# Kernel optimization log

Hardware: AMD Instinct MI355X
Metric: run time of the kernel (lower is better)

## Reference

```python
import jax, jax.numpy as jnp
import numpy as np

B = 1024
IN_Q = 2048
IN_KV = 2048
NH = 16
D = 64
INNER = NH * D
TF = 4
NC = 2
EPS = 1e-5
SLOPE = 0.01  # LeakyReLU default negative slope


def setup_inputs() -> dict:
    key = jax.random.key(0)
    ks = jax.random.split(key, 8)
    s = 0.02
    return {
        "q_input": jax.random.normal(ks[0], (B, IN_Q), jnp.float32),
        "kv_input": jax.random.normal(ks[1], (B, IN_KV), jnp.float32),
        "Wq": jax.random.normal(ks[2], (INNER, IN_Q), jnp.float32) * s,
        "bq": jax.random.normal(ks[3], (INNER,), jnp.float32) * s,
        "Wkv": jax.random.normal(ks[4], (2 * INNER, IN_KV), jnp.float32) * s,
        "bkv": jax.random.normal(ks[5], (2 * INNER,), jnp.float32) * s,
        "bn_w": jnp.ones((TF,), jnp.float32),
        "bn_b": jnp.zeros((TF,), jnp.float32),
        "Wo": jax.random.normal(ks[6], (NC, TF), jnp.float32) * s,
        "bo": jax.random.normal(ks[7], (NC,), jnp.float32) * s,
    }


def reference(q_input, kv_input, Wq, bq, Wkv, bkv, bn_w, bn_b, Wo, bo):
    b = q_input.shape[0]
    # projections: [B, NH, D] and [B, NH, 2D]
    q = (q_input @ Wq.T + bq).reshape(b, NH, D)
    kv = (kv_input @ Wkv.T + bkv).reshape(b, NH, 2 * D)
    k, v = kv[..., :D], kv[..., D:]
    # sim[b,n] = k[b,n,:] . q[b,n,:]  (per-head scalar score)
    sim = jnp.einsum("bnd,bnd->bn", k, q)
    att = jax.nn.softmax(sim, axis=-1)  # softmax over heads
    # torch.matmul([B,NH], [B,NH,D]) broadcast -> out[i,j,:] = sum_n att[j,n] v[i,n,:]
    att_out = jnp.einsum("jn,ind->ijd", att, v)  # [B, B, D]
    flat = att_out.reshape(b, b * D)  # [B, B*D]
    # AdaptiveAvgPool1d to TF bins (L % TF == 0 -> exact reshape-mean)
    pooled = flat.reshape(b, TF, (b * D) // TF).mean(axis=-1)  # [B, TF]
    x = jnp.where(pooled >= 0, pooled, SLOPE * pooled)  # LeakyReLU
    # BatchNorm1d, train mode (batch stats, biased variance)
    mean = x.mean(axis=0)
    var = x.var(axis=0)
    x = (x - mean) * jax.lax.rsqrt(var + EPS) * bn_w + bn_b
    # dropout(p=0.0) is identity
    return x @ Wo.T + bo  # [B, NC]
```

## Files before the change

### kernel.cpp

```cpp
#include <hip/hip_runtime.h>
#include <hip/hip_bf16.h>

#define EPS 1e-5f
#define SLOPE 0.01f

typedef __attribute__((ext_vector_type(8))) short bfrag8;
typedef __attribute__((ext_vector_type(4))) float f32x4;

#define AS1 __attribute__((address_space(1)))
#define AS3 __attribute__((address_space(3)))

#define WS_SIM_OFF   0u
#define WS_S_OFF     65536u
#define WS_WVS_OFF   131072u
#define WS_BVS_OFF   262144u
#define WS_AIMG_OFF  262208u
#define WS_BIMG_OFF  8650816u

__device__ __forceinline__ unsigned short f2bf(float f) {
    union { float f; unsigned int u; } x; x.f = f;
    unsigned int r = (x.u + 0x7FFFu + ((x.u >> 16) & 1u)) >> 16;
    return (unsigned short)r;
}
__device__ __forceinline__ uint4 pack8(const float4& a, const float4& b) {
    uint4 r;
    r.x = (unsigned)f2bf(a.x) | ((unsigned)f2bf(a.y) << 16);
    r.y = (unsigned)f2bf(a.z) | ((unsigned)f2bf(a.w) << 16);
    r.z = (unsigned)f2bf(b.x) | ((unsigned)f2bf(b.y) << 16);
    r.w = (unsigned)f2bf(b.z) | ((unsigned)f2bf(b.w) << 16);
    return r;
}

#define PREP_A    524288
#define PREP_B2   (PREP_A + 524288)
#define PREP_WVSE (PREP_B2 + 32768)
#define PREP_SIMZ (PREP_WVSE + 16384)
#define PREP_END  (PREP_SIMZ + 16)

__global__ __launch_bounds__(256) void prep_kernel(
        const float* __restrict__ qin, const float* __restrict__ kvin,
        const float* __restrict__ Wq, const float* __restrict__ Wkv,
        const float* __restrict__ bkv, unsigned char* __restrict__ ws) {
    int gid = blockIdx.x * 256 + threadIdx.x;
    if (gid < PREP_A) {
        int p  = gid & 511;
        int kt = (gid >> 9) & 31;
        int mt = (gid >> 14) & 15;
        int s2 = gid >> 18;
        int rit = p >> 3;
        int gk = (p & 7) ^ (rit & 7);
        int row = mt * 64 + rit;
        int k = kt * 64 + gk * 8;
        const float* src = (s2 ? kvin : qin) + (size_t)row * 2048 + k;
        float4 v0 = *(const float4*)src;
        float4 v1 = *(const float4*)(src + 4);
        *(uint4*)(ws + WS_AIMG_OFF + (size_t)gid * 16) = pack8(v0, v1);
    } else if (gid < PREP_B2) {
        int g2 = gid - PREP_A;
        int p  = g2 & 511;
        int kt = (g2 >> 9) & 31;
        int dh = (g2 >> 14) & 1;
        int h  = g2 >> 15;
        int cit = p >> 3;
        int gk = (p & 7) ^ (cit & 7);
        int k = kt * 64 + gk * 8;
        const float* wrow;
        if (cit < 32) wrow = Wq  + (size_t)(h * 64 + dh * 32 + cit) * 2048;
        else          wrow = Wkv + (size_t)(h * 128 + dh * 32 + (cit - 32)) * 2048;
        float4 v0 = *(const float4*)(wrow + k);
        float4 v1 = *(const float4*)(wrow + k + 4);
        *(uint4*)(ws + WS_BIMG_OFF + (size_t)g2 * 16) = pack8(v0, v1);
    } else if (gid < PREP_WVSE) {
        int g2 = gid - PREP_B2;
        int n = g2 >> 11, c = g2 & 2047;
        const float* base = Wkv + (size_t)(n * 128 + 64) * 2048 + c;
        float s = 0.f;
        #pragma unroll 8
        for (int d = 0; d < 64; ++d) s += base[(size_t)d * 2048];
        ((float*)(ws + WS_WVS_OFF))[c * 16 + n] = s;
    } else if (gid < PREP_SIMZ) {
        ((float*)(ws + WS_SIM_OFF))[gid - PREP_WVSE] = 0.f;
    } else if (gid < PREP_END) {
        int n = gid - PREP_SIMZ;
        float b = 0.f;
        #pragma unroll
        for (int d = 0; d < 64; ++d) b += bkv[n * 128 + 64 + d];
        ((float*)(ws + WS_BVS_OFF))[n] = b;
    }
}

__global__ __launch_bounds__(512, 1) void gemm_sim_kernel(unsigned char* __restrict__ ws,
        const float* __restrict__ bq, const float* __restrict__ bkv) {
    __shared__ alignas(16) unsigned short LAq[3][4096];
    __shared__ alignas(16) unsigned short LAkv[3][4096];
    __shared__ alignas(16) unsigned short LB[3][2][4096];

    const int t = threadIdx.x;
    const int w = t >> 6, l = t & 63;
    const int hp = blockIdx.x, mt = blockIdx.y, dh = blockIdx.z;
    const int qk = w >> 2, hh = (w >> 1) & 1, wr = w & 1;
    const int h = hp * 2 + hh;
    const int lrow = l & 15, lhi = l >> 4;
    const int m0 = mt * 64;

    const unsigned char* aqBase = ws + WS_AIMG_OFF + (size_t)mt * 262144u;
    const unsigned char* akBase = aqBase + 4194304u;
    const unsigned char* bBase0 = ws + WS_BIMG_OFF + (size_t)((hp * 2 + 0) * 2 + dh) * 262144u;
    const unsigned char* bBase1 = ws + WS_BIMG_OFF + (size_t)((hp * 2 + 1) * 2 + dh) * 262144u;
    float* sim = (float*)(ws + WS_SIM_OFF);

    int offA[2][2], offB[2][2];
    #pragma unroll
    for (int ks = 0; ks < 2; ++ks)
        #pragma unroll
        for (int i = 0; i < 2; ++i) {
            int r = wr * 32 + i * 16 + lrow;
            int c = qk * 32 + i * 16 + lrow;
            offA[ks][i] = r * 128 + (((ks * 4 + lhi) ^ (r & 7)) << 4);
            offB[ks][i] = c * 128 + (((ks * 4 + lhi) ^ (c & 7)) << 4);
        }

    f32x4 acc00 = (f32x4)0.f, acc01 = (f32x4)0.f, acc10 = (f32x4)0.f, acc11 = (f32x4)0.f;

#define STAGE(kt_, buf_) do {                                                        \
    const unsigned char* _aq = aqBase + (size_t)(kt_) * 8192 + t * 16;               \
    const unsigned char* _ak = akBase + (size_t)(kt_) * 8192 + t * 16;               \
    const unsigned char* _b0 = bBase0 + (size_t)(kt_) * 8192 + t * 16;               \
    const unsigned char* _b1 = bBase1 + (size_t)(kt_) * 8192 + t * 16;               \
    unsigned char* _dq = ((unsigned char*)&LAq[0][0])  + (size_t)(buf_) * 8192 + t * 16;  \
    unsigned char* _dk = ((unsigned char*)&LAkv[0][0]) + (size_t)(buf_) * 8192 + t * 16;  \
    unsigned char* _d0 = ((unsigned char*)&LB[0][0][0]) + (size_t)(buf_) * 16384 + t * 16;        \
    unsigned char* _d1 = ((unsigned char*)&LB[0][0][0]) + (size_t)(buf_) * 16384 + 8192 + t * 16; \
    __builtin_amdgcn_global_load_lds((const AS1 unsigned int*)(const void*)_aq,      \
        (AS3 unsigned int*)(void*)_dq, 16, 0, 0);                                    \
    __builtin_amdgcn_global_load_lds((const AS1 unsigned int*)(const void*)_ak,      \
        (AS3 unsigned int*)(void*)_dk, 16, 0, 0);                                    \
    __builtin_amdgcn_global_load_lds((const AS1 unsigned int*)(const void*)_b0,      \
        (AS3 unsigned int*)(void*)_d0, 16, 0, 0);                                    \
    __builtin_amdgcn_global_load_lds((const AS1 unsigned int*)(const void*)_b1,      \
        (AS3 unsigned int*)(void*)_d1, 16, 0, 0);                                    \
    } while (0)

    STAGE(0, 0);
    STAGE(1, 1);
    asm volatile("s_waitcnt vmcnt(4)" ::: "memory");
    __builtin_amdgcn_sched_barrier(0);
    __builtin_amdgcn_s_barrier();
    __builtin_amdgcn_sched_barrier(0);

    int cur = 0, nxt = 2;
    for (int kt = 0; kt < 32; ++kt) {
        {
            const char* Ab = (const char*)(qk ? &LAkv[0][0] : &LAq[0][0]) + cur * 8192;
            const char* Bb = (const char*)&LB[0][0][0] + cur * 16384 + hh * 8192;
            #pragma unroll
            for (int ks = 0; ks < 2; ++ks) {
                bfrag8 fa0 = *(const bfrag8*)(Ab + offA[ks][0]);
                bfrag8 fa1 = *(const bfrag8*)(Ab + offA[ks][1]);
                bfrag8 fb0 = *(const bfrag8*)(Bb + offB[ks][0]);
                bfrag8 fb1 = *(const bfrag8*)(Bb + offB[ks][1]);
                acc00 = __builtin_amdgcn_mfma_f32_16x16x32_bf16(fa0, fb0, acc00, 0, 0, 0);
                acc01 = __builtin_amdgcn_mfma_f32_16x16x32_bf16(fa0, fb1, acc01, 0, 0, 0);
                acc10 = __builtin_amdgcn_mfma_f32_16x16x32_bf16(fa1, fb0, acc10, 0, 0, 0);
                acc11 = __builtin_amdgcn_mfma_f32_16x16x32_bf16(fa1, fb1, acc11, 0, 0, 0);
            }
        }
        if (kt < 30) {
            STAGE(kt + 2, nxt);
            asm volatile("s_waitcnt vmcnt(4)" ::: "memory");
        } else {
            asm volatile("s_waitcnt vmcnt(0)" ::: "memory");
        }
        __builtin_amdgcn_sched_barrier(0);
        __builtin_amdgcn_s_barrier();
        __builtin_amdgcn_sched_barrier(0);
        cur = (cur == 2) ? 0 : cur + 1;
        nxt = (nxt == 2) ? 0 : nxt + 1;
    }
#undef STAGE

    f32x4 acc[2][2] = {{acc00, acc01}, {acc10, acc11}};
    float biasv[2];
    #pragma unroll
    for (int ni = 0; ni < 2; ++ni) {
        int d = dh * 32 + ni * 16 + lrow;
        biasv[ni] = qk ? bkv[h * 128 + d] : bq[h * 64 + d];
    }
    #pragma unroll
    for (int mi = 0; mi < 2; ++mi)
        #pragma unroll
        for (int ni = 0; ni < 2; ++ni)
            #pragma unroll
            for (int r = 0; r < 4; ++r)
                acc[mi][ni][r] += biasv[ni];

    float* cqs = (float*)&LAq[0][0];
    if (!qk) {
        #pragma unroll
        for (int mi = 0; mi < 2; ++mi)
            #pragma unroll
            for (int ni = 0; ni < 2; ++ni)
                #pragma unroll
                for (int r = 0; r < 4; ++r) {
                    int row = mi * 16 + lhi * 4 + r;
                    cqs[(((hh * 2 + wr) * 32 + row) * 32) + ni * 16 + lrow] = acc[mi][ni][r];
                }
    }
    __syncthreads();
    if (qk) {
        #pragma unroll
        for (int mi = 0; mi < 2; ++mi) {
            float pv[4];
            #pragma unroll
            for (int r = 0; r < 4; ++r) {
                int row = mi * 16 + lhi * 4 + r;
                const float* crow = cqs + ((hh * 2 + wr) * 32 + row) * 32;
                pv[r] = crow[lrow] * acc[mi][0][r] + crow[16 + lrow] * acc[mi][1][r];
            }
            #pragma unroll
            for (int r = 0; r < 4; ++r) {
                float v = pv[r];
                v += __shfl_xor(v, 1); v += __shfl_xor(v, 2);
                v += __shfl_xor(v, 4); v += __shfl_xor(v, 8);
                if ((l & 15) == 0) {
                    int row = wr * 32 + mi * 16 + (l >> 4) * 4 + r;
                    atomicAdd(&sim[(m0 + row) * 16 + h], v);
                }
            }
        }
    }
}

__global__ __launch_bounds__(256) void s_kernel(
        const float* __restrict__ kvin, unsigned char* __restrict__ ws) {
    int b = blockIdx.x, t = threadIdx.x;
    int w = t >> 6, l = t & 63;
    __shared__ float SW[4][16];
    int n = t & 15, g = t >> 4;
    const float* kvrow = kvin + (size_t)b * 2048;
    const float* wv = (const float*)(ws + WS_WVS_OFF);
    float p = 0.f;
    #pragma unroll 4
    for (int tt = 0; tt < 128; ++tt) {
        int c = g + (tt << 4);
        p = fmaf(kvrow[c], wv[c * 16 + n], p);
    }
    p += __shfl_xor(p, 16);
    p += __shfl_xor(p, 32);
    if (l < 16) SW[w][n] = p;
    __syncthreads();
    if (t < 16) {
        float sv = SW[0][t] + SW[1][t] + SW[2][t] + SW[3][t]
                 + ((const float*)(ws + WS_BVS_OFF))[t];
        ((float*)(ws + WS_S_OFF))[b * 16 + t] = sv;
    }
}

__global__ __launch_bounds__(1024) void final_kernel(
        const float* __restrict__ bn_w, const float* __restrict__ bn_b,
        const float* __restrict__ Wo, const float* __restrict__ bo,
        const unsigned char* __restrict__ ws, float* __restrict__ out) {
    int t = threadIdx.x;
    int w = t >> 6;
    int l = t & 63;
    __shared__ float Aw[16][16];
    __shared__ float Af[4][16];
    __shared__ float SWs[16][8];
    __shared__ float FS[8];
    __shared__ float sc[4], sh[4];

    float a16[16];
    {
        const float* srow = (const float*)(ws + WS_SIM_OFF) + (size_t)t * 16;
        float4 v0 = *(const float4*)(srow + 0);
        float4 v1 = *(const float4*)(srow + 4);
        float4 v2 = *(const float4*)(srow + 8);
        float4 v3 = *(const float4*)(srow + 12);
        a16[0]=v0.x; a16[1]=v0.y; a16[2]=v0.z; a16[3]=v0.w;
        a16[4]=v1.x; a16[5]=v1.y; a16[6]=v1.z; a16[7]=v1.w;
        a16[8]=v2.x; a16[9]=v2.y; a16[10]=v2.z; a16[11]=v2.w;
        a16[12]=v3.x; a16[13]=v3.y; a16[14]=v3.z; a16[15]=v3.w;
        float m = a16[0];
        #pragma unroll
        for (int n = 1; n < 16; ++n) m = fmaxf(m, a16[n]);
        float den = 0.f;
        #pragma unroll
        for (int n = 0; n < 16; ++n) { a16[n] = expf(a16[n] - m); den += a16[n]; }
        float inv = 1.f / den;
        #pragma unroll
        for (int n = 0; n < 16; ++n) a16[n] *= inv;
    }
    #pragma unroll
    for (int n = 0; n < 16; ++n) {
        float p = a16[n];
        p += __shfl_xor(p, 1);  p += __shfl_xor(p, 2);
        p += __shfl_xor(p, 4);  p += __shfl_xor(p, 8);
        p += __shfl_xor(p, 16); p += __shfl_xor(p, 32);
        a16[n] = p;
    }
    if (l == 0) {
        #pragma unroll
        for (int n = 0; n < 16; ++n) Aw[w][n] = a16[n];
    }
    __syncthreads();
    if (t < 64) {
        int f = t >> 4, n = t & 15;
        Af[f][n] = Aw[4*f][n] + Aw[4*f+1][n] + Aw[4*f+2][n] + Aw[4*f+3][n];
    }
    __syncthreads();

    float sv[16];
    {
        const float* srow = (const float*)(ws + WS_S_OFF) + (size_t)t * 16;
        float4 v0 = *(const float4*)(srow + 0);
        float4 v1 = *(const float4*)(srow + 4);
        float4 v2 = *(const float4*)(srow + 8);
        float4 v3 = *(const float4*)(srow + 12);
        sv[0]=v0.x; sv[1]=v0.y; sv[2]=v0.z; sv[3]=v0.w;
        sv[4]=v1.x; sv[5]=v1.y; sv[6]=v1.z; sv[7]=v1.w;
        sv[8]=v2.x; sv[9]=v2.y; sv[10]=v2.z; sv[11]=v2.w;
        sv[12]=v3.x; sv[13]=v3.y; sv[14]=v3.z; sv[15]=v3.w;
    }
    float x[4];
    #pragma unroll
    for (int f = 0; f < 4; ++f) {
        float p = 0.f;
        #pragma unroll
        for (int n = 0; n < 16; ++n) p = fmaf(Af[f][n], sv[n], p);
        p *= (1.f / 16384.f);
        x[f] = (p >= 0.f) ? p : SLOPE * p;
    }

    float st[8];
    #pragma unroll
    for (int f = 0; f < 4; ++f) { st[f] = x[f]; st[4 + f] = x[f] * x[f]; }
    #pragma unroll
    for (int j = 0; j < 8; ++j) {
        float p = st[j];
        p += __shfl_xor(p, 1);  p += __shfl_xor(p, 2);
        p += __shfl_xor(p, 4);  p += __shfl_xor(p, 8);
        p += __shfl_xor(p, 16); p += __shfl_xor(p, 32);
        st[j] = p;
    }
    if (l == 0) {
        #pragma unroll
        for (int j = 0; j < 8; ++j) SWs[w][j] = st[j];
    }
    __syncthreads();
    if (t < 8) {
        float p = 0.f;
        #pragma unroll
        for (int ww = 0; ww < 16; ++ww) p += SWs[ww][t];
        FS[t] = p;
    }
    __syncthreads();
    if (t < 4) {
        float mean = FS[t] * (1.f / 1024.f);
        float var  = FS[4 + t] * (1.f / 1024.f) - mean * mean;
        float s = bn_w[t] / sqrtf(var + EPS);
        sc[t] = s;
        sh[t] = bn_b[t] - mean * s;
    }
    __syncthreads();

    float o0 = bo[0], o1 = bo[1];
    #pragma unroll
    for (int f = 0; f < 4; ++f) {
        float xh = x[f] * sc[f] + sh[f];
        o0 = fmaf(xh, Wo[f], o0);
        o1 = fmaf(xh, Wo[4 + f], o1);
    }
    *(float2*)(out + (size_t)t * 2) = make_float2(o0, o1);
}

extern "C" void kernel_launch(void* const* d_in, const int* in_sizes, int n_in,
                              void* d_out, int out_size, void* d_ws, size_t ws_size,
                              hipStream_t stream) {
    const float* q_input  = (const float*)d_in[0];
    const float* kv_input = (const float*)d_in[1];
    const float* Wq   = (const float*)d_in[2];
    const float* bq   = (const float*)d_in[3];
    const float* Wkv  = (const float*)d_in[4];
    const float* bkv  = (const float*)d_in[5];
    const float* bn_w = (const float*)d_in[6];
    const float* bn_b = (const float*)d_in[7];
    const float* Wo   = (const float*)d_in[8];
    const float* bo   = (const float*)d_in[9];
    float* out = (float*)d_out;
    unsigned char* ws = (unsigned char*)d_ws;

    hipLaunchKernelGGL(prep_kernel, dim3((PREP_END + 255) / 256), dim3(256), 0, stream,
                       q_input, kv_input, Wq, Wkv, bkv, ws);
    hipLaunchKernelGGL(gemm_sim_kernel, dim3(8, 16, 2), dim3(512), 0, stream,
                       ws, bq, bkv);
    hipLaunchKernelGGL(s_kernel, dim3(1024), dim3(256), 0, stream, kv_input, ws);
    hipLaunchKernelGGL(final_kernel, dim3(1), dim3(1024), 0, stream,
                       bn_w, bn_b, Wo, bo, ws, out);
}
```

Baseline: 59.74 us.

## Fuse activation bf16 conversion into GEMM loader, dropping prep A-image pass

The prep kernel no longer converts q_input/kv_input into a swizzled bf16 image in workspace. Instead the GEMM kernel loads fp32 activations straight from global memory into registers, converts them with v_cvt_pk_bf16_f32 and writes them into swizzled LDS, using a 2-stage register/LDS pipeline for A and keeping the 3-stage direct-to-LDS path for B. This removes an extra global write and read of the activation image. In exchange the GEMM reads fp32 (twice the bytes), and each A tile is re-read by the 16 blocks that share it. The launch bounds also drop the min-blocks hint.

New measurement: 70.05 us. +17.2%, slower.

```diff
diff --git a/kernel.cpp b/kernel.cpp
--- a/kernel.cpp
+++ b/kernel.cpp
@@ -14,8 +14,7 @@
 #define WS_S_OFF     65536u
 #define WS_WVS_OFF   131072u
 #define WS_BVS_OFF   262144u
-#define WS_AIMG_OFF  262208u
-#define WS_BIMG_OFF  8650816u
+#define WS_BIMG_OFF  262208u
 
 __device__ __forceinline__ unsigned short f2bf(float f) {
     union { float f; unsigned int u; } x; x.f = f;
@@ -30,37 +29,26 @@
     r.w = (unsigned)f2bf(b.z) | ((unsigned)f2bf(b.w) << 16);
     return r;
 }
-
-#define PREP_A    524288
-#define PREP_B2   (PREP_A + 524288)
+__device__ __forceinline__ unsigned cvtpk(float lo, float hi) {
+    unsigned r;
+    asm("v_cvt_pk_bf16_f32 %0, %1, %2" : "=v"(r) : "v"(lo), "v"(hi));
+    return r;
+}
+
+#define PREP_B2   524288
 #define PREP_WVSE (PREP_B2 + 32768)
 #define PREP_SIMZ (PREP_WVSE + 16384)
 #define PREP_END  (PREP_SIMZ + 16)
 
 __global__ __launch_bounds__(256) void prep_kernel(
-        const float* __restrict__ qin, const float* __restrict__ kvin,
         const float* __restrict__ Wq, const float* __restrict__ Wkv,
         const float* __restrict__ bkv, unsigned char* __restrict__ ws) {
     int gid = blockIdx.x * 256 + threadIdx.x;
-    if (gid < PREP_A) {
+    if (gid < PREP_B2) {
         int p  = gid & 511;
         int kt = (gid >> 9) & 31;
-        int mt = (gid >> 14) & 15;
-        int s2 = gid >> 18;
-        int rit = p >> 3;
-        int gk = (p & 7) ^ (rit & 7);
-        int row = mt * 64 + rit;
-        int k = kt * 64 + gk * 8;
-        const float* src = (s2 ? kvin : qin) + (size_t)row * 2048 + k;
-        float4 v0 = *(const float4*)src;
-        float4 v1 = *(const float4*)(src + 4);
-        *(uint4*)(ws + WS_AIMG_OFF + (size_t)gid * 16) = pack8(v0, v1);
-    } else if (gid < PREP_B2) {
-        int g2 = gid - PREP_A;
-        int p  = g2 & 511;
-        int kt = (g2 >> 9) & 31;
-        int dh = (g2 >> 14) & 1;
-        int h  = g2 >> 15;
+        int dh = (gid >> 14) & 1;
+        int h  = gid >> 15;
         int cit = p >> 3;
         int gk = (p & 7) ^ (cit & 7);
         int k = kt * 64 + gk * 8;
@@ -69,7 +57,7 @@
         else          wrow = Wkv + (size_t)(h * 128 + dh * 32 + (cit - 32)) * 2048;
         float4 v0 = *(const float4*)(wrow + k);
         float4 v1 = *(const float4*)(wrow + k + 4);
-        *(uint4*)(ws + WS_BIMG_OFF + (size_t)g2 * 16) = pack8(v0, v1);
+        *(uint4*)(ws + WS_BIMG_OFF + (size_t)gid * 16) = pack8(v0, v1);
     } else if (gid < PREP_WVSE) {
         int g2 = gid - PREP_B2;
         int n = g2 >> 11, c = g2 & 2047;
@@ -89,10 +77,12 @@
     }
 }
 
-__global__ __launch_bounds__(512, 1) void gemm_sim_kernel(unsigned char* __restrict__ ws,
+__global__ __launch_bounds__(512) void gemm_sim_kernel(
+        const float* __restrict__ qin, const float* __restrict__ kvin,
+        unsigned char* __restrict__ ws,
         const float* __restrict__ bq, const float* __restrict__ bkv) {
-    __shared__ alignas(16) unsigned short LAq[3][4096];
-    __shared__ alignas(16) unsigned short LAkv[3][4096];
+    __shared__ alignas(16) unsigned short LAq[2][4096];
+    __shared__ alignas(16) unsigned short LAkv[2][4096];
     __shared__ alignas(16) unsigned short LB[3][2][4096];
 
     const int t = threadIdx.x;
@@ -103,11 +93,17 @@
     const int lrow = l & 15, lhi = l >> 4;
     const int m0 = mt * 64;
 
-    const unsigned char* aqBase = ws + WS_AIMG_OFF + (size_t)mt * 262144u;
-    const unsigned char* akBase = aqBase + 4194304u;
     const unsigned char* bBase0 = ws + WS_BIMG_OFF + (size_t)((hp * 2 + 0) * 2 + dh) * 262144u;
     const unsigned char* bBase1 = ws + WS_BIMG_OFF + (size_t)((hp * 2 + 1) * 2 + dh) * 262144u;
     float* sim = (float*)(ws + WS_SIM_OFF);
+
+    const int ish = t >> 8, tt = t & 255;
+    const int arow = tt >> 2, aq4 = tt & 3;
+    const int gk0 = aq4 * 2, gk1 = gk0 + 1;
+    const float* aSrc = (ish ? kvin : qin) + (size_t)(m0 + arow) * 2048;
+    const int adst0 = arow * 128 + ((gk0 ^ (arow & 7)) << 4);
+    const int adst1 = arow * 128 + ((gk1 ^ (arow & 7)) << 4);
+    unsigned char* aDst = (unsigned char*)(ish ? &LAkv[0][0] : &LAq[0][0]);
 
     int offA[2][2], offB[2][2];
     #pragma unroll
@@ -122,62 +118,80 @@
 
     f32x4 acc00 = (f32x4)0.f, acc01 = (f32x4)0.f, acc10 = (f32x4)0.f, acc11 = (f32x4)0.f;
 
-#define STAGE(kt_, buf_) do {                                                        \
-    const unsigned char* _aq = aqBase + (size_t)(kt_) * 8192 + t * 16;               \
-    const unsigned char* _ak = akBase + (size_t)(kt_) * 8192 + t * 16;               \
-    const unsigned char* _b0 = bBase0 + (size_t)(kt_) * 8192 + t * 16;               \
-    const unsigned char* _b1 = bBase1 + (size_t)(kt_) * 8192 + t * 16;               \
-    unsigned char* _dq = ((unsigned char*)&LAq[0][0])  + (size_t)(buf_) * 8192 + t * 16;  \
-    unsigned char* _dk = ((unsigned char*)&LAkv[0][0]) + (size_t)(buf_) * 8192 + t * 16;  \
+#define LOAD_A(kt_, S) do {                                                   \
+    S[0] = *(const float4*)(aSrc + (kt_) * 64 + gk0 * 8);                     \
+    S[1] = *(const float4*)(aSrc + (kt_) * 64 + gk0 * 8 + 4);                 \
+    S[2] = *(const float4*)(aSrc + (kt_) * 64 + gk1 * 8);                     \
+    S[3] = *(const float4*)(aSrc + (kt_) * 64 + gk1 * 8 + 4); } while (0)
+
+#define WRITE_A(S, buf_) do {                                                 \
+    uint4 _u0, _u1;                                                           \
+    _u0.x = cvtpk(S[0].x, S[0].y); _u0.y = cvtpk(S[0].z, S[0].w);             \
+    _u0.z = cvtpk(S[1].x, S[1].y); _u0.w = cvtpk(S[1].z, S[1].w);             \
+    _u1.x = cvtpk(S[2].x, S[2].y); _u1.y = cvtpk(S[2].z, S[2].w);             \
+    _u1.z = cvtpk(S[3].x, S[3].y); _u1.w = cvtpk(S[3].z, S[3].w);             \
+    *(uint4*)(aDst + (buf_) * 8192 + adst0) = _u0;                            \
+    *(uint4*)(aDst + (buf_) * 8192 + adst1) = _u1; } while (0)
+
+#define STAGE_B(kt_, buf_) do {                                               \
+    const unsigned char* _b0 = bBase0 + (size_t)(kt_) * 8192 + t * 16;        \
+    const unsigned char* _b1 = bBase1 + (size_t)(kt_) * 8192 + t * 16;        \
     unsigned char* _d0 = ((unsigned char*)&LB[0][0][0]) + (size_t)(buf_) * 16384 + t * 16;        \
     unsigned char* _d1 = ((unsigned char*)&LB[0][0][0]) + (size_t)(buf_) * 16384 + 8192 + t * 16; \
-    __builtin_amdgcn_global_load_lds((const AS1 unsigned int*)(const void*)_aq,      \
-        (AS3 unsigned int*)(void*)_dq, 16, 0, 0);                                    \
-    __builtin_amdgcn_global_load_lds((const AS1 unsigned int*)(const void*)_ak,      \
-        (AS3 unsigned int*)(void*)_dk, 16, 0, 0);                                    \
-    __builtin_amdgcn_global_load_lds((const AS1 unsigned int*)(const void*)_b0,      \
-        (AS3 unsigned int*)(void*)_d0, 16, 0, 0);                                    \
-    __builtin_amdgcn_global_load_lds((const AS1 unsigned int*)(const void*)_b1,      \
-        (AS3 unsigned int*)(void*)_d1, 16, 0, 0);                                    \
-    } while (0)
-
-    STAGE(0, 0);
-    STAGE(1, 1);
-    asm volatile("s_waitcnt vmcnt(4)" ::: "memory");
-    __builtin_amdgcn_sched_barrier(0);
-    __builtin_amdgcn_s_barrier();
-    __builtin_amdgcn_sched_barrier(0);
-
-    int cur = 0, nxt = 2;
-    for (int kt = 0; kt < 32; ++kt) {
-        {
-            const char* Ab = (const char*)(qk ? &LAkv[0][0] : &LAq[0][0]) + cur * 8192;
-            const char* Bb = (const char*)&LB[0][0][0] + cur * 16384 + hh * 8192;
-            #pragma unroll
-            for (int ks = 0; ks < 2; ++ks) {
-                bfrag8 fa0 = *(const bfrag8*)(Ab + offA[ks][0]);
-                bfrag8 fa1 = *(const bfrag8*)(Ab + offA[ks][1]);
-                bfrag8 fb0 = *(const bfrag8*)(Bb + offB[ks][0]);
-                bfrag8 fb1 = *(const bfrag8*)(Bb + offB[ks][1]);
-                acc00 = __builtin_amdgcn_mfma_f32_16x16x32_bf16(fa0, fb0, acc00, 0, 0, 0);
-                acc01 = __builtin_amdgcn_mfma_f32_16x16x32_bf16(fa0, fb1, acc01, 0, 0, 0);
-                acc10 = __builtin_amdgcn_mfma_f32_16x16x32_bf16(fa1, fb0, acc10, 0, 0, 0);
-                acc11 = __builtin_amdgcn_mfma_f32_16x16x32_bf16(fa1, fb1, acc11, 0, 0, 0);
-            }
+    __builtin_amdgcn_global_load_lds((const AS1 unsigned int*)(const void*)_b0,  \
+        (AS3 unsigned int*)(void*)_d0, 16, 0, 0);                             \
+    __builtin_amdgcn_global_load_lds((const AS1 unsigned int*)(const void*)_b1,  \
+        (AS3 unsigned int*)(void*)_d1, 16, 0, 0); } while (0)
+
+#define COMPUTE(kt_) do {                                                     \
+    const char* Ab = (const char*)(qk ? &LAkv[0][0] : &LAq[0][0]) + ((kt_) & 1) * 8192; \
+    const char* Bb = (const char*)&LB[0][0][0] + ((kt_) % 3) * 16384 + hh * 8192;       \
+    _Pragma("unroll")                                                         \
+    for (int _ks = 0; _ks < 2; ++_ks) {                                       \
+        bfrag8 fa0 = *(const bfrag8*)(Ab + offA[_ks][0]);                     \
+        bfrag8 fa1 = *(const bfrag8*)(Ab + offA[_ks][1]);                     \
+        bfrag8 fb0 = *(const bfrag8*)(Bb + offB[_ks][0]);                     \
+        bfrag8 fb1 = *(const bfrag8*)(Bb + offB[_ks][1]);                     \
+        acc00 = __builtin_amdgcn_mfma_f32_16x16x32_bf16(fa0, fb0, acc00, 0, 0, 0); \
+        acc01 = __builtin_amdgcn_mfma_f32_16x16x32_bf16(fa0, fb1, acc01, 0, 0, 0); \
+        acc10 = __builtin_amdgcn_mfma_f32_16x16x32_bf16(fa1, fb0, acc10, 0, 0, 0); \
+        acc11 = __builtin_amdgcn_mfma_f32_16x16x32_bf16(fa1, fb1, acc11, 0, 0, 0); \
+    } } while (0)
+
+#define BARRIER_V(n_) do {                                                    \
+    asm volatile("s_waitcnt vmcnt(" #n_ ")" ::: "memory");                    \
+    asm volatile("s_waitcnt lgkmcnt(0)" ::: "memory");                        \
+    __builtin_amdgcn_sched_barrier(0);                                        \
+    __builtin_amdgcn_s_barrier();                                             \
+    __builtin_amdgcn_sched_barrier(0); } while (0)
+
+    float4 E[4], O[4];
+
+    LOAD_A(0, E);
+    WRITE_A(E, 0);
+    STAGE_B(0, 0);
+    STAGE_B(1, 1);
+    LOAD_A(1, O);
+    BARRIER_V(6);
+
+    for (int j = 0; j < 16; ++j) {
+        const int kt = 2 * j;
+        if (j < 15) { LOAD_A(kt + 2, E); STAGE_B(kt + 2, (kt + 2) % 3); }
+        COMPUTE(kt);
+        WRITE_A(O, (kt + 1) & 1);
+        if (j < 15) BARRIER_V(6); else BARRIER_V(0);
+        if (j < 15) { LOAD_A(kt + 3, O); STAGE_B(kt + 3, (kt + 3) % 3); }
+        COMPUTE(kt + 1);
+        if (j < 15) {
+            WRITE_A(E, kt & 1);
+            BARRIER_V(6);
         }
-        if (kt < 30) {
-            STAGE(kt + 2, nxt);
-            asm volatile("s_waitcnt vmcnt(4)" ::: "memory");
-        } else {
-            asm volatile("s_waitcnt vmcnt(0)" ::: "memory");
-        }
-        __builtin_amdgcn_sched_barrier(0);
-        __builtin_amdgcn_s_barrier();
-        __builtin_amdgcn_sched_barrier(0);
-        cur = (cur == 2) ? 0 : cur + 1;
-        nxt = (nxt == 2) ? 0 : nxt + 1;
-    }
-#undef STAGE
+    }
+#undef LOAD_A
+#undef WRITE_A
+#undef STAGE_B
+#undef COMPUTE
+#undef BARRIER_V
 
     f32x4 acc[2][2] = {{acc00, acc01}, {acc10, acc11}};
     float biasv[2];
@@ -195,6 +209,7 @@
                 acc[mi][ni][r] += biasv[ni];
 
     float* cqs = (float*)&LAq[0][0];
+    __syncthreads();
     if (!qk) {
         #pragma unroll
         for (int mi = 0; mi < 2; ++mi)
@@ -390,9 +405,9 @@
     unsigned char* ws = (unsigned char*)d_ws;
 
     hipLaunchKernelGGL(prep_kernel, dim3((PREP_END + 255) / 256), dim3(256), 0, stream,
-                       q_input, kv_input, Wq, Wkv, bkv, ws);
+                       Wq, Wkv, bkv, ws);
     hipLaunchKernelGGL(gemm_sim_kernel, dim3(8, 16, 2), dim3(512), 0, stream,
-                       ws, bq, bkv);
+                       q_input, kv_input, ws, bq, bkv);
     hipLaunchKernelGGL(s_kernel, dim3(1024), dim3(256), 0, stream, kv_input, ws);
     hipLaunchKernelGGL(final_kernel, dim3(1), dim3(1024), 0, stream,
                        bn_w, bn_b, Wo, bo, ws, out);
```

## Restructure GEMM pipeline to double-buffered two-k-tile stages with fewer barriers

Applied to the files above, without the earlier changes.

Replaces the triple-buffered one-k-tile-per-iteration loop with a double-buffered loop in which each stage holds two k-tiles. Loads for the next two tiles are issued before computing the current pair, and one full vmcnt(0) wait and barrier follow each pair. This halves the number of workgroup barriers per k-loop. In exchange, LDS use rises and the wait now drains all outstanding loads each iteration instead of keeping one stage in flight.

Result: slower. 63.77 us (+6.7%).

```diff
diff --git a/kernel.cpp b/kernel.cpp
--- a/kernel.cpp
+++ b/kernel.cpp
@@ -91,9 +91,9 @@
 
 __global__ __launch_bounds__(512, 1) void gemm_sim_kernel(unsigned char* __restrict__ ws,
         const float* __restrict__ bq, const float* __restrict__ bkv) {
-    __shared__ alignas(16) unsigned short LAq[3][4096];
-    __shared__ alignas(16) unsigned short LAkv[3][4096];
-    __shared__ alignas(16) unsigned short LB[3][2][4096];
+    __shared__ alignas(16) unsigned short LAq[2][2][4096];
+    __shared__ alignas(16) unsigned short LAkv[2][2][4096];
+    __shared__ alignas(16) unsigned short LB[2][2][2][4096];
 
     const int t = threadIdx.x;
     const int w = t >> 6, l = t & 63;
@@ -122,15 +122,15 @@
 
     f32x4 acc00 = (f32x4)0.f, acc01 = (f32x4)0.f, acc10 = (f32x4)0.f, acc11 = (f32x4)0.f;
 
-#define STAGE(kt_, buf_) do {                                                        \
+#define STAGE1(kt_, buf_, sub_) do {                                                 \
     const unsigned char* _aq = aqBase + (size_t)(kt_) * 8192 + t * 16;               \
     const unsigned char* _ak = akBase + (size_t)(kt_) * 8192 + t * 16;               \
     const unsigned char* _b0 = bBase0 + (size_t)(kt_) * 8192 + t * 16;               \
     const unsigned char* _b1 = bBase1 + (size_t)(kt_) * 8192 + t * 16;               \
-    unsigned char* _dq = ((unsigned char*)&LAq[0][0])  + (size_t)(buf_) * 8192 + t * 16;  \
-    unsigned char* _dk = ((unsigned char*)&LAkv[0][0]) + (size_t)(buf_) * 8192 + t * 16;  \
-    unsigned char* _d0 = ((unsigned char*)&LB[0][0][0]) + (size_t)(buf_) * 16384 + t * 16;        \
-    unsigned char* _d1 = ((unsigned char*)&LB[0][0][0]) + (size_t)(buf_) * 16384 + 8192 + t * 16; \
+    unsigned char* _dq = ((unsigned char*)&LAq[0][0][0])  + (size_t)((buf_) * 2 + (sub_)) * 8192 + t * 16; \
+    unsigned char* _dk = ((unsigned char*)&LAkv[0][0][0]) + (size_t)((buf_) * 2 + (sub_)) * 8192 + t * 16; \
+    unsigned char* _d0 = ((unsigned char*)&LB[0][0][0][0]) + (size_t)((buf_) * 2 + (sub_)) * 16384 + t * 16;        \
+    unsigned char* _d1 = ((unsigned char*)&LB[0][0][0][0]) + (size_t)((buf_) * 2 + (sub_)) * 16384 + 8192 + t * 16; \
     __builtin_amdgcn_global_load_lds((const AS1 unsigned int*)(const void*)_aq,      \
         (AS3 unsigned int*)(void*)_dq, 16, 0, 0);                                    \
     __builtin_amdgcn_global_load_lds((const AS1 unsigned int*)(const void*)_ak,      \
@@ -141,43 +141,44 @@
         (AS3 unsigned int*)(void*)_d1, 16, 0, 0);                                    \
     } while (0)
 
-    STAGE(0, 0);
-    STAGE(1, 1);
-    asm volatile("s_waitcnt vmcnt(4)" ::: "memory");
+#define COMPUTE(buf_, sub_) do {                                                     \
+    const char* Ab = (const char*)(qk ? &LAkv[0][0][0] : &LAq[0][0][0])              \
+                   + ((buf_) * 2 + (sub_)) * 8192;                                   \
+    const char* Bb = (const char*)&LB[0][0][0][0] + ((buf_) * 2 + (sub_)) * 16384 + hh * 8192; \
+    _Pragma("unroll")                                                                \
+    for (int ks = 0; ks < 2; ++ks) {                                                 \
+        bfrag8 fa0 = *(const bfrag8*)(Ab + offA[ks][0]);                             \
+        bfrag8 fa1 = *(const bfrag8*)(Ab + offA[ks][1]);                             \
+        bfrag8 fb0 = *(const bfrag8*)(Bb + offB[ks][0]);                             \
+        bfrag8 fb1 = *(const bfrag8*)(Bb + offB[ks][1]);                             \
+        acc00 = __builtin_amdgcn_mfma_f32_16x16x32_bf16(fa0, fb0, acc00, 0, 0, 0);   \
+        acc01 = __builtin_amdgcn_mfma_f32_16x16x32_bf16(fa0, fb1, acc01, 0, 0, 0);   \
+        acc10 = __builtin_amdgcn_mfma_f32_16x16x32_bf16(fa1, fb0, acc10, 0, 0, 0);   \
+        acc11 = __builtin_amdgcn_mfma_f32_16x16x32_bf16(fa1, fb1, acc11, 0, 0, 0);   \
+    } } while (0)
+
+    STAGE1(0, 0, 0);
+    STAGE1(1, 0, 1);
+    asm volatile("s_waitcnt vmcnt(0)" ::: "memory");
     __builtin_amdgcn_sched_barrier(0);
     __builtin_amdgcn_s_barrier();
     __builtin_amdgcn_sched_barrier(0);
 
-    int cur = 0, nxt = 2;
-    for (int kt = 0; kt < 32; ++kt) {
-        {
-            const char* Ab = (const char*)(qk ? &LAkv[0][0] : &LAq[0][0]) + cur * 8192;
-            const char* Bb = (const char*)&LB[0][0][0] + cur * 16384 + hh * 8192;
-            #pragma unroll
-            for (int ks = 0; ks < 2; ++ks) {
-                bfrag8 fa0 = *(const bfrag8*)(Ab + offA[ks][0]);
-                bfrag8 fa1 = *(const bfrag8*)(Ab + offA[ks][1]);
-                bfrag8 fb0 = *(const bfrag8*)(Bb + offB[ks][0]);
-                bfrag8 fb1 = *(const bfrag8*)(Bb + offB[ks][1]);
-                acc00 = __builtin_amdgcn_mfma_f32_16x16x32_bf16(fa0, fb0, acc00, 0, 0, 0);
-                acc01 = __builtin_amdgcn_mfma_f32_16x16x32_bf16(fa0, fb1, acc01, 0, 0, 0);
-                acc10 = __builtin_amdgcn_mfma_f32_16x16x32_bf16(fa1, fb0, acc10, 0, 0, 0);
-                acc11 = __builtin_amdgcn_mfma_f32_16x16x32_bf16(fa1, fb1, acc11, 0, 0, 0);
-            }
+    for (int p = 0; p < 16; ++p) {
+        const int buf = p & 1;
+        if (p < 15) {
+            STAGE1(2 * p + 2, buf ^ 1, 0);
+            STAGE1(2 * p + 3, buf ^ 1, 1);
         }
-        if (kt < 30) {
-            STAGE(kt + 2, nxt);
-            asm volatile("s_waitcnt vmcnt(4)" ::: "memory");
-        } else {
-            asm volatile("s_waitcnt vmcnt(0)" ::: "memory");
-        }
+        COMPUTE(buf, 0);
+        COMPUTE(buf, 1);
+        asm volatile("s_waitcnt vmcnt(0)" ::: "memory");
         __builtin_amdgcn_sched_barrier(0);
         __builtin_amdgcn_s_barrier();
         __builtin_amdgcn_sched_barrier(0);
-        cur = (cur == 2) ? 0 : cur + 1;
-        nxt = (nxt == 2) ? 0 : nxt + 1;
-    }
-#undef STAGE
+    }
+#undef STAGE1
+#undef COMPUTE
 
     f32x4 acc[2][2] = {{acc00, acc01}, {acc10, acc11}};
     float biasv[2];
@@ -194,7 +195,7 @@
             for (int r = 0; r < 4; ++r)
                 acc[mi][ni][r] += biasv[ni];
 
-    float* cqs = (float*)&LAq[0][0];
+    float* cqs = (float*)&LAq[0][0][0];
     if (!qk) {
         #pragma unroll
         for (int mi = 0; mi < 2; ++mi)
```
